# Performance work log

Hardware: AMD Instinct MI355X
Metric: run time of the kernel (lower is better)

Reference implementation:

```python
import jax, jax.numpy as jnp
import numpy as np

G, D, H, O = 8, 1024, 2048, 1024

def _xavier(key, shape):
    # xavier_normal_ on nn.Linear weight [out, in]: std = sqrt(2/(fan_in+fan_out))
    fan_out, fan_in = shape[-2], shape[-1]
    std = float(np.sqrt(2.0 / (fan_in + fan_out)))
    return jax.random.normal(key, shape, dtype=jnp.float32) * std

def setup_inputs() -> dict:
    key = jax.random.key(0)
    kx, kg, ku, kd = jax.random.split(key, 4)
    x = jax.random.normal(kx, (65536, D), dtype=jnp.float32)
    # weights stored per-group in nn.Linear layout [out, in]
    Wg = _xavier(kg, (G, H, D))
    Wu = _xavier(ku, (G, H, D))
    Wd = _xavier(kd, (G, O, H))
    return {"x": x, "Wg": Wg, "Wu": Wu, "Wd": Wd}

def reference(x, Wg, Wu, Wd):
    # x: [B*G, D] -> [B, G, D]
    xb = x.reshape(-1, G, D)
    gate = jnp.einsum('bgd,ghd->bgh', xb, Wg)   # [B, G, H]
    up = jnp.einsum('bgd,ghd->bgh', xb, Wu)     # [B, G, H]
    hidden = jax.nn.silu(gate) * up             # fused SwiGLU
    out = jnp.einsum('bgh,goh->bgo', hidden, Wd)  # [B, G, O]
    return out.reshape(-1, O)
```

## Files before the change

kernel.cpp:

```cpp
#include <hip/hip_runtime.h>


#define GN 8
#define DN 1024
#define HN 2048
#define ON 1024

typedef __attribute__((ext_vector_type(8))) short short8;
typedef __attribute__((ext_vector_type(4))) float f32x4;
typedef __attribute__((ext_vector_type(4))) unsigned int u32x4;

#define BARR() __builtin_amdgcn_s_barrier()
#define WAIT_LGKM0()                                       \
  do {                                                     \
    asm volatile("s_waitcnt lgkmcnt(0)" ::: "memory");     \
    __builtin_amdgcn_sched_barrier(0);                     \
  } while (0)

#define DS128(dst, base, imm)                                                  \
  asm volatile("ds_read_b128 %0, %1 offset:" #imm                              \
               : "=v"(dst)                                                     \
               : "v"((const __attribute__((address_space(3))) unsigned short*)(base)))

__device__ __forceinline__ void async16(const void* g, void* l) {
  __builtin_amdgcn_global_load_lds(
      (const __attribute__((address_space(1))) void*)g,
      (__attribute__((address_space(3))) void*)l, 16, 0, 0);
}

__device__ __forceinline__ unsigned short f2bf(float f) {
  unsigned int u = __float_as_uint(f);
  u += 0x7FFFu + ((u >> 16) & 1u);
  return (unsigned short)(u >> 16);
}

__global__ __launch_bounds__(256) void cvt_f32_bf16(
    const float* __restrict__ in, unsigned short* __restrict__ out, int n) {
  int t = blockIdx.x * 256 + threadIdx.x;
  int i = t * 8;
  if (i >= n) return;
  f32x4 a = *(const f32x4*)(in + i);
  f32x4 b = *(const f32x4*)(in + i + 4);
  u32x4 r;
  r.x = (unsigned)f2bf(a.x) | ((unsigned)f2bf(a.y) << 16);
  r.y = (unsigned)f2bf(a.z) | ((unsigned)f2bf(a.w) << 16);
  r.z = (unsigned)f2bf(b.x) | ((unsigned)f2bf(b.y) << 16);
  r.w = (unsigned)f2bf(b.z) | ((unsigned)f2bf(b.w) << 16);
  *(u32x4*)(out + i) = r;
}

__global__ __launch_bounds__(512, 2) void gemm1_swiglu(
    const unsigned short* __restrict__ Xb, const unsigned short* __restrict__ Wgb,
    const unsigned short* __restrict__ Wub, unsigned short* __restrict__ Hid) {
  extern __shared__ unsigned short sm[];
  unsigned short* sA = sm;
  unsigned short* sG = sm + 32768;
  unsigned short* sU = sm + 49152;

  const int bid = blockIdx.x;
  const int g = bid >> 5;
  const int n0 = ((bid >> 1) & 15) * 128;
  const int mh = bid & 1;

  const int tid = threadIdx.x;
  const int lane = tid & 63;
  const int w = tid >> 6;
  const int wm = w >> 2, wn = w & 3;
  const int fr = lane & 15, fc = lane >> 4;
  const int sR = (fc + ((fr >> 1) & 3)) & 3;

  const unsigned short* aBase[2];
  unsigned short* aDst[2];
#pragma unroll
  for (int j = 0; j < 2; ++j) {
    int R = j * 128 + w * 16 + (lane >> 2);
    int c = ((lane & 3) - ((R >> 1) & 3)) & 3;
    aBase[j] = Xb + ((size_t)((mh * 4096 + R) * 8 + g)) * DN + c * 8;
    aDst[j] = &sA[(j * 128 + w * 16) * 32];
  }
  const unsigned short *gSrc, *uSrc;
  unsigned short *gDst, *uDst;
  {
    int R = w * 16 + (lane >> 2);
    int c = ((lane & 3) - ((R >> 1) & 3)) & 3;
    gSrc = Wgb + ((size_t)(g * HN + n0 + R)) * DN + c * 8;
    uSrc = Wub + ((size_t)(g * HN + n0 + R)) * DN + c * 8;
    gDst = &sG[(w * 16) * 32];
    uDst = &sU[(w * 16) * 32];
  }

  auto stageA = [&](int Tg, int kk) {
    const int buf = (Tg & 1) * 2 + kk;
    const size_t toff = (size_t)(Tg >> 4) * (256u * 8u * DN);
    const int ko = (Tg & 15) * 64 + kk * 32;
#pragma unroll
    for (int j = 0; j < 2; ++j)
      async16(aBase[j] + toff + ko, aDst[j] + buf * 8192);
  };
  auto stageB = [&](int Tg, int kk) {
    const int buf = (Tg & 1) * 2 + kk;
    const int ko = (Tg & 15) * 64 + kk * 32;
    async16(gSrc + ko, gDst + buf * 4096);
    async16(uSrc + ko, uDst + buf * 4096);
  };
  auto readA = [&](int Tg, int kk, short8* a) {
    const unsigned short* p =
        sA + ((Tg & 1) * 2 + kk) * 8192 + (wm * 128 + fr) * 32 + sR * 8;
    DS128(a[0], p, 0);
    DS128(a[1], p, 1024);
    DS128(a[2], p, 2048);
    DS128(a[3], p, 3072);
    DS128(a[4], p, 4096);
    DS128(a[5], p, 5120);
    DS128(a[6], p, 6144);
    DS128(a[7], p, 7168);
  };
  auto readB = [&](const unsigned short* base, int Tg, int kk, short8* b) {
    const unsigned short* p =
        base + ((Tg & 1) * 2 + kk) * 4096 + (wn * 32 + fr) * 32 + sR * 8;
    DS128(b[0], p, 0);
    DS128(b[1], p, 1024);
  };

  f32x4 accg[8][2], accu[8][2];
#pragma unroll
  for (int mi = 0; mi < 8; ++mi)
#pragma unroll
    for (int ni = 0; ni < 2; ++ni) {
      accg[mi][ni] = (f32x4)(0.0f);
      accu[mi][ni] = (f32x4)(0.0f);
    }

  auto mm16 = [&](const short8* a, const short8* b, f32x4(*acc)[2]) {
    __builtin_amdgcn_s_setprio(1);
#pragma unroll
    for (int mi = 0; mi < 8; ++mi)
#pragma unroll
      for (int ni = 0; ni < 2; ++ni)
        acc[mi][ni] = __builtin_amdgcn_mfma_f32_16x16x32_bf16(
            a[mi], b[ni], acc[mi][ni], 0, 0, 0);
    __builtin_amdgcn_s_setprio(0);
  };

  stageA(0, 0); stageB(0, 0); stageA(0, 1); stageB(0, 1);
  stageA(1, 0); stageB(1, 0); stageA(1, 1);
  asm volatile("s_waitcnt vmcnt(6)" ::: "memory");
  BARR();

  short8 af[8], bg[2], bu[2];
  const int q = lane >> 4, cl = lane & 15;
  const int NIT = 128;
#pragma unroll 1
  for (int it = 0; it < NIT; ++it) {
    const int T = 2 * it;
    const bool full = (it + 1 < NIT);
    readA(T, 0, af); readB(sG, T, 0, bg);
    stageB(T + 1, 1);
    BARR();
    WAIT_LGKM0();
    mm16(af, bg, accg);
    BARR();
    readB(sU, T, 0, bu);
    if (full) stageA(T + 2, 0);
    BARR();
    WAIT_LGKM0();
    mm16(af, bu, accu);
    BARR();
    readA(T, 1, af); readB(sG, T, 1, bg);
    if (full) stageB(T + 2, 0);
    BARR();
    WAIT_LGKM0();
    mm16(af, bg, accg);
    BARR();
    readB(sU, T, 1, bu);
    if (full) stageA(T + 2, 1);
    BARR();
    WAIT_LGKM0();
    mm16(af, bu, accu);
    if (full) { asm volatile("s_waitcnt vmcnt(6)" ::: "memory"); }
    else      { asm volatile("s_waitcnt vmcnt(0)" ::: "memory"); }
    BARR();
    readA(T + 1, 0, af); readB(sG, T + 1, 0, bg);
    if (full) stageB(T + 2, 1);
    BARR();
    WAIT_LGKM0();
    mm16(af, bg, accg);
    BARR();
    readB(sU, T + 1, 0, bu);
    if (full) stageA(T + 3, 0);
    BARR();
    WAIT_LGKM0();
    mm16(af, bu, accu);
    BARR();
    readA(T + 1, 1, af); readB(sG, T + 1, 1, bg);
    if (full) stageB(T + 3, 0);
    BARR();
    WAIT_LGKM0();
    mm16(af, bg, accg);
    BARR();
    readB(sU, T + 1, 1, bu);
    if (full) stageA(T + 3, 1);
    BARR();
    WAIT_LGKM0();
    mm16(af, bu, accu);
    if (full) { asm volatile("s_waitcnt vmcnt(6)" ::: "memory"); }
    BARR();
    if ((T & 15) == 14) {
      const int tile = T >> 4;
      const int m0 = (mh * 16 + tile) * 256;
#pragma unroll
      for (int mi = 0; mi < 8; ++mi)
#pragma unroll
        for (int ni = 0; ni < 2; ++ni) {
          int hcol = n0 + wn * 32 + ni * 16 + cl;
#pragma unroll
          for (int i2 = 0; i2 < 4; ++i2) {
            int b = m0 + wm * 128 + mi * 16 + q * 4 + i2;
            float gf = accg[mi][ni][i2];
            float uf = accu[mi][ni][i2];
            float hv = (gf / (1.0f + __expf(-gf))) * uf;
            Hid[((size_t)(b * 8 + g)) * HN + hcol] = f2bf(hv);
          }
          accg[mi][ni] = (f32x4)(0.0f);
          accu[mi][ni] = (f32x4)(0.0f);
        }
    }
  }
}

__global__ __launch_bounds__(512, 2) void gemm2_down(
    const unsigned short* __restrict__ Hid, const unsigned short* __restrict__ Wdb,
    float* __restrict__ Out) {
  extern __shared__ unsigned short sm[];
  unsigned short* sA = sm;
  unsigned short* sB = sm + 32768;

  const int bid = blockIdx.x;
  const int g = bid >> 5;
  const int n0 = ((bid >> 3) & 3) * 256;
  const int mq = bid & 7;

  const int tid = threadIdx.x;
  const int lane = tid & 63;
  const int w = tid >> 6;
  const int wm = w >> 2, wn = w & 3;
  const int fr = lane & 15, fc = lane >> 4;
  const int sR = (fc + ((fr >> 1) & 3)) & 3;

  const unsigned short* aBase[2];
  const unsigned short* bSrc[2];
  unsigned short* aDst[2];
  unsigned short* bDst[2];
#pragma unroll
  for (int j = 0; j < 2; ++j) {
    int R = j * 128 + w * 16 + (lane >> 2);
    int c = ((lane & 3) - ((R >> 1) & 3)) & 3;
    aBase[j] = Hid + ((size_t)((mq * 1024 + R) * 8 + g)) * HN + c * 8;
    bSrc[j] = Wdb + ((size_t)(g * ON + n0 + R)) * HN + c * 8;
    aDst[j] = &sA[(j * 128 + w * 16) * 32];
    bDst[j] = &sB[(j * 128 + w * 16) * 32];
  }

  auto stageA = [&](int Tg, int kk) {
    const int buf = (Tg & 1) * 2 + kk;
    const size_t toff = (size_t)(Tg >> 5) * (256u * 8u * HN);
    const int ko = (Tg & 31) * 64 + kk * 32;
#pragma unroll
    for (int j = 0; j < 2; ++j)
      async16(aBase[j] + toff + ko, aDst[j] + buf * 8192);
  };
  auto stageB = [&](int Tg, int kk) {
    const int buf = (Tg & 1) * 2 + kk;
    const int ko = (Tg & 31) * 64 + kk * 32;
#pragma unroll
    for (int j = 0; j < 2; ++j) async16(bSrc[j] + ko, bDst[j] + buf * 8192);
  };
  auto readA = [&](int Tg, int kk, short8* a) {
    const unsigned short* p =
        sA + ((Tg & 1) * 2 + kk) * 8192 + (wm * 128 + fr) * 32 + sR * 8;
    DS128(a[0], p, 0);
    DS128(a[1], p, 1024);
    DS128(a[2], p, 2048);
    DS128(a[3], p, 3072);
    DS128(a[4], p, 4096);
    DS128(a[5], p, 5120);
    DS128(a[6], p, 6144);
    DS128(a[7], p, 7168);
  };
  auto readB = [&](int Tg, int kk, int nb, short8* b) {
    const unsigned short* p =
        sB + ((Tg & 1) * 2 + kk) * 8192 + (wn * 64 + nb * 16 + fr) * 32 + sR * 8;
    DS128(b[0], p, 0);
    DS128(b[1], p, 1024);
  };

  f32x4 acc[8][4];
#pragma unroll
  for (int mi = 0; mi < 8; ++mi)
#pragma unroll
    for (int ni = 0; ni < 4; ++ni) acc[mi][ni] = (f32x4)(0.0f);

  auto mm16 = [&](const short8* a, const short8* b, int nb) {
    __builtin_amdgcn_s_setprio(1);
#pragma unroll
    for (int mi = 0; mi < 8; ++mi)
#pragma unroll
      for (int nj = 0; nj < 2; ++nj)
        acc[mi][nb + nj] = __builtin_amdgcn_mfma_f32_16x16x32_bf16(
            a[mi], b[nj], acc[mi][nb + nj], 0, 0, 0);
    __builtin_amdgcn_s_setprio(0);
  };

  stageA(0, 0); stageB(0, 0); stageA(0, 1); stageB(0, 1);
  stageA(1, 0); stageB(1, 0); stageA(1, 1);
  asm volatile("s_waitcnt vmcnt(6)" ::: "memory");
  BARR();

  short8 af[8], bf[2];
  const int q = lane >> 4, cl = lane & 15;
  const int NIT = 64;
#pragma unroll 1
  for (int it = 0; it < NIT; ++it) {
    const int T = 2 * it;
    const bool full = (it + 1 < NIT);
    readA(T, 0, af); readB(T, 0, 0, bf);
    stageB(T + 1, 1);
    BARR();
    WAIT_LGKM0();
    mm16(af, bf, 0);
    BARR();
    readB(T, 0, 2, bf);
    if (full) stageA(T + 2, 0);
    BARR();
    WAIT_LGKM0();
    mm16(af, bf, 2);
    BARR();
    readA(T, 1, af); readB(T, 1, 0, bf);
    if (full) stageB(T + 2, 0);
    BARR();
    WAIT_LGKM0();
    mm16(af, bf, 0);
    BARR();
    readB(T, 1, 2, bf);
    if (full) stageA(T + 2, 1);
    BARR();
    WAIT_LGKM0();
    mm16(af, bf, 2);
    if (full) { asm volatile("s_waitcnt vmcnt(6)" ::: "memory"); }
    else      { asm volatile("s_waitcnt vmcnt(0)" ::: "memory"); }
    BARR();
    readA(T + 1, 0, af); readB(T + 1, 0, 0, bf);
    if (full) stageB(T + 2, 1);
    BARR();
    WAIT_LGKM0();
    mm16(af, bf, 0);
    BARR();
    readB(T + 1, 0, 2, bf);
    if (full) stageA(T + 3, 0);
    BARR();
    WAIT_LGKM0();
    mm16(af, bf, 2);
    BARR();
    readA(T + 1, 1, af); readB(T + 1, 1, 0, bf);
    if (full) stageB(T + 3, 0);
    BARR();
    WAIT_LGKM0();
    mm16(af, bf, 0);
    BARR();
    readB(T + 1, 1, 2, bf);
    if (full) stageA(T + 3, 1);
    BARR();
    WAIT_LGKM0();
    mm16(af, bf, 2);
    if (full) { asm volatile("s_waitcnt vmcnt(6)" ::: "memory"); }
    BARR();
    if ((T & 31) == 30) {
      const int tile = T >> 5;
      const int m0 = (mq * 4 + tile) * 256;
#pragma unroll
      for (int mi = 0; mi < 8; ++mi)
#pragma unroll
        for (int ni = 0; ni < 4; ++ni) {
          int o = n0 + wn * 64 + ni * 16 + cl;
#pragma unroll
          for (int i2 = 0; i2 < 4; ++i2) {
            int b = m0 + wm * 128 + mi * 16 + q * 4 + i2;
            Out[((size_t)(b * 8 + g)) * ON + o] = acc[mi][ni][i2];
          }
          acc[mi][ni] = (f32x4)(0.0f);
        }
    }
  }
}

extern "C" void kernel_launch(void* const* d_in, const int* in_sizes, int n_in,
                              void* d_out, int out_size, void* d_ws, size_t ws_size,
                              hipStream_t stream) {
  const float* x  = (const float*)d_in[0];
  const float* Wg = (const float*)d_in[1];
  const float* Wu = (const float*)d_in[2];
  const float* Wd = (const float*)d_in[3];
  float* out = (float*)d_out;

  const int NX = 65536 * 1024;
  const int NW = GN * HN * DN;

  unsigned short* xb = (unsigned short*)d_ws;
  unsigned short* wg = xb + (size_t)NX;
  unsigned short* wu = wg + (size_t)NW;
  unsigned short* wd = wu + (size_t)NW;
  unsigned short* hid = wd + (size_t)NW;

  static bool once = false;
  if (!once) {
    hipFuncSetAttribute((const void*)gemm1_swiglu,
                        hipFuncAttributeMaxDynamicSharedMemorySize, 131072);
    hipFuncSetAttribute((const void*)gemm2_down,
                        hipFuncAttributeMaxDynamicSharedMemorySize, 131072);
    once = true;
  }

  cvt_f32_bf16<<<NX / 8 / 256, 256, 0, stream>>>(x, xb, NX);
  cvt_f32_bf16<<<NW / 8 / 256, 256, 0, stream>>>(Wg, wg, NW);
  cvt_f32_bf16<<<NW / 8 / 256, 256, 0, stream>>>(Wu, wu, NW);
  cvt_f32_bf16<<<NW / 8 / 256, 256, 0, stream>>>(Wd, wd, NW);

  gemm1_swiglu<<<dim3(256), dim3(512), 131072, stream>>>(xb, wg, wu, hid);
  gemm2_down<<<dim3(256), dim3(512), 131072, stream>>>(hid, wd, out);
}
```

Before: 1.356 ms.

## Software-pipeline LDS fragment reads with double-buffered registers and fewer barriers

Both GEMM kernels now double-buffer A fragments in registers (af0/af1). Each MFMA block overlaps with the LDS reads for the next step, using partial lgkmcnt waits instead of a full drain, and the main loop runs one barrier per phase instead of two. Global-to-LDS staging waits now use vmcnt(8) per phase, and tail staging is guarded inside the stage lambdas. The block-index mapping is also changed so neighbouring blocks share the same weight tile across groups and halves, which may improve L2 reuse. The cost is more register pressure from the extra fragment buffers and a tighter hazard protocol around LDS buffer reuse.

Measured after the change: 1.564 ms. 15.3% more time.

```diff
diff --git a/kernel.cpp b/kernel.cpp
--- a/kernel.cpp
+++ b/kernel.cpp
@@ -11,11 +11,13 @@
 typedef __attribute__((ext_vector_type(4))) unsigned int u32x4;
 
 #define BARR() __builtin_amdgcn_s_barrier()
-#define WAIT_LGKM0()                                       \
-  do {                                                     \
-    asm volatile("s_waitcnt lgkmcnt(0)" ::: "memory");     \
-    __builtin_amdgcn_sched_barrier(0);                     \
+#define SCHED0() __builtin_amdgcn_sched_barrier(0)
+#define LGKM(n)                                                \
+  do {                                                         \
+    asm volatile("s_waitcnt lgkmcnt(" #n ")" ::: "memory");    \
+    __builtin_amdgcn_sched_barrier(0);                         \
   } while (0)
+#define VM8() asm volatile("s_waitcnt vmcnt(8)" ::: "memory")
 
 #define DS128(dst, base, imm)                                                  \
   asm volatile("ds_read_b128 %0, %1 offset:" #imm                              \
@@ -58,9 +60,9 @@
   unsigned short* sU = sm + 49152;
 
   const int bid = blockIdx.x;
-  const int g = bid >> 5;
-  const int n0 = ((bid >> 1) & 15) * 128;
+  const int g = (bid & 15) >> 1;
   const int mh = bid & 1;
+  const int n0 = (bid >> 4) * 128;
 
   const int tid = threadIdx.x;
   const int lane = tid & 63;
@@ -89,35 +91,40 @@
     uDst = &sU[(w * 16) * 32];
   }
 
-  auto stageA = [&](int Tg, int kk) {
-    const int buf = (Tg & 1) * 2 + kk;
-    const size_t toff = (size_t)(Tg >> 4) * (256u * 8u * DN);
-    const int ko = (Tg & 15) * 64 + kk * 32;
-#pragma unroll
-    for (int j = 0; j < 2; ++j)
-      async16(aBase[j] + toff + ko, aDst[j] + buf * 8192);
-  };
-  auto stageB = [&](int Tg, int kk) {
-    const int buf = (Tg & 1) * 2 + kk;
-    const int ko = (Tg & 15) * 64 + kk * 32;
+  auto stageA = [&](int t, int kk) {
+    if (t >= 256) return;
+    const int buf = (t & 1) * 2 + kk;
+    const size_t off = (size_t)(t >> 4) * (256u * 8u * DN) + (t & 15) * 64 + kk * 32;
+#pragma unroll
+    for (int j = 0; j < 2; ++j) async16(aBase[j] + off, aDst[j] + buf * 8192);
+  };
+  auto stageB = [&](int t, int kk) {
+    if (t >= 256) return;
+    const int buf = (t & 1) * 2 + kk;
+    const int ko = (t & 15) * 64 + kk * 32;
     async16(gSrc + ko, gDst + buf * 4096);
     async16(uSrc + ko, uDst + buf * 4096);
   };
-  auto readA = [&](int Tg, int kk, short8* a) {
-    const unsigned short* p =
-        sA + ((Tg & 1) * 2 + kk) * 8192 + (wm * 128 + fr) * 32 + sR * 8;
+  auto aPtr = [&](int t, int kk) {
+    return sA + ((t & 1) * 2 + kk) * 8192 + (wm * 128 + fr) * 32 + sR * 8;
+  };
+  auto readAlo = [&](int t, int kk, short8* a) {
+    const unsigned short* p = aPtr(t, kk);
     DS128(a[0], p, 0);
     DS128(a[1], p, 1024);
     DS128(a[2], p, 2048);
     DS128(a[3], p, 3072);
+  };
+  auto readAhi = [&](int t, int kk, short8* a) {
+    const unsigned short* p = aPtr(t, kk);
     DS128(a[4], p, 4096);
     DS128(a[5], p, 5120);
     DS128(a[6], p, 6144);
     DS128(a[7], p, 7168);
   };
-  auto readB = [&](const unsigned short* base, int Tg, int kk, short8* b) {
+  auto readB = [&](const unsigned short* base, int t, int kk, short8* b) {
     const unsigned short* p =
-        base + ((Tg & 1) * 2 + kk) * 4096 + (wn * 32 + fr) * 32 + sR * 8;
+        base + ((t & 1) * 2 + kk) * 4096 + (wn * 32 + fr) * 32 + sR * 8;
     DS128(b[0], p, 0);
     DS128(b[1], p, 1024);
   };
@@ -144,70 +151,66 @@
 
   stageA(0, 0); stageB(0, 0); stageA(0, 1); stageB(0, 1);
   stageA(1, 0); stageB(1, 0); stageA(1, 1);
-  asm volatile("s_waitcnt vmcnt(6)" ::: "memory");
+  asm volatile("s_waitcnt vmcnt(10)" ::: "memory");
   BARR();
-
-  short8 af[8], bg[2], bu[2];
+  short8 af0[8], af1[8], bg[2], bu[2];
+  readAlo(0, 0, af0); readAhi(0, 0, af0); readB(sG, 0, 0, bg);
+
   const int q = lane >> 4, cl = lane & 15;
   const int NIT = 128;
 #pragma unroll 1
   for (int it = 0; it < NIT; ++it) {
     const int T = 2 * it;
-    const bool full = (it + 1 < NIT);
-    readA(T, 0, af); readB(sG, T, 0, bg);
+    BARR(); SCHED0();
     stageB(T + 1, 1);
-    BARR();
-    WAIT_LGKM0();
-    mm16(af, bg, accg);
-    BARR();
-    readB(sU, T, 0, bu);
-    if (full) stageA(T + 2, 0);
-    BARR();
-    WAIT_LGKM0();
-    mm16(af, bu, accu);
-    BARR();
-    readA(T, 1, af); readB(sG, T, 1, bg);
-    if (full) stageB(T + 2, 0);
-    BARR();
-    WAIT_LGKM0();
-    mm16(af, bg, accg);
-    BARR();
-    readB(sU, T, 1, bu);
-    if (full) stageA(T + 2, 1);
-    BARR();
-    WAIT_LGKM0();
-    mm16(af, bu, accu);
-    if (full) { asm volatile("s_waitcnt vmcnt(6)" ::: "memory"); }
-    else      { asm volatile("s_waitcnt vmcnt(0)" ::: "memory"); }
-    BARR();
-    readA(T + 1, 0, af); readB(sG, T + 1, 0, bg);
-    if (full) stageB(T + 2, 1);
-    BARR();
-    WAIT_LGKM0();
-    mm16(af, bg, accg);
-    BARR();
-    readB(sU, T + 1, 0, bu);
-    if (full) stageA(T + 3, 0);
-    BARR();
-    WAIT_LGKM0();
-    mm16(af, bu, accu);
-    BARR();
-    readA(T + 1, 1, af); readB(sG, T + 1, 1, bg);
-    if (full) stageB(T + 3, 0);
-    BARR();
-    WAIT_LGKM0();
-    mm16(af, bg, accg);
-    BARR();
-    readB(sU, T + 1, 1, bu);
-    if (full) stageA(T + 3, 1);
-    BARR();
-    WAIT_LGKM0();
-    mm16(af, bu, accu);
-    if (full) { asm volatile("s_waitcnt vmcnt(6)" ::: "memory"); }
-    BARR();
+    readB(sU, T, 0, bu); readAlo(T, 1, af1);
+    LGKM(6);
+    mm16(af0, bg, accg);
+    VM8();
+    BARR(); SCHED0();
+    stageA(T + 2, 0);
+    readAhi(T, 1, af1); readB(sG, T, 1, bg);
+    LGKM(6);
+    mm16(af0, bu, accu);
+    VM8();
+    BARR(); SCHED0();
+    stageB(T + 2, 0);
+    readB(sU, T, 1, bu); readAlo(T + 1, 0, af0);
+    LGKM(6);
+    mm16(af1, bg, accg);
+    VM8();
+    BARR(); SCHED0();
+    stageA(T + 2, 1);
+    readAhi(T + 1, 0, af0); readB(sG, T + 1, 0, bg);
+    LGKM(6);
+    mm16(af1, bu, accu);
+    VM8();
+    BARR(); SCHED0();
+    stageB(T + 2, 1);
+    readB(sU, T + 1, 0, bu); readAlo(T + 1, 1, af1);
+    LGKM(6);
+    mm16(af0, bg, accg);
+    VM8();
+    BARR(); SCHED0();
+    stageA(T + 3, 0);
+    readAhi(T + 1, 1, af1); readB(sG, T + 1, 1, bg);
+    LGKM(6);
+    mm16(af0, bu, accu);
+    VM8();
+    BARR(); SCHED0();
+    stageB(T + 3, 0);
+    readB(sU, T + 1, 1, bu); readAlo(T + 2, 0, af0);
+    LGKM(6);
+    mm16(af1, bg, accg);
+    VM8();
+    BARR(); SCHED0();
+    stageA(T + 3, 1);
+    readAhi(T + 2, 0, af0); readB(sG, T + 2, 0, bg);
+    LGKM(6);
+    mm16(af1, bu, accu);
+    VM8();
     if ((T & 15) == 14) {
-      const int tile = T >> 4;
-      const int m0 = (mh * 16 + tile) * 256;
+      const int m0 = (mh * 16 + (T >> 4)) * 256;
 #pragma unroll
       for (int mi = 0; mi < 8; ++mi)
 #pragma unroll
@@ -236,9 +239,9 @@
   unsigned short* sB = sm + 32768;
 
   const int bid = blockIdx.x;
-  const int g = bid >> 5;
-  const int n0 = ((bid >> 3) & 3) * 256;
+  const int g = (bid & 63) >> 3;
   const int mq = bid & 7;
+  const int n0 = (bid >> 6) * 256;
 
   const int tid = threadIdx.x;
   const int lane = tid & 63;
@@ -261,35 +264,40 @@
     bDst[j] = &sB[(j * 128 + w * 16) * 32];
   }
 
-  auto stageA = [&](int Tg, int kk) {
-    const int buf = (Tg & 1) * 2 + kk;
-    const size_t toff = (size_t)(Tg >> 5) * (256u * 8u * HN);
-    const int ko = (Tg & 31) * 64 + kk * 32;
-#pragma unroll
-    for (int j = 0; j < 2; ++j)
-      async16(aBase[j] + toff + ko, aDst[j] + buf * 8192);
-  };
-  auto stageB = [&](int Tg, int kk) {
-    const int buf = (Tg & 1) * 2 + kk;
-    const int ko = (Tg & 31) * 64 + kk * 32;
+  auto stageA = [&](int t, int kk) {
+    if (t >= 128) return;
+    const int buf = (t & 1) * 2 + kk;
+    const size_t off = (size_t)(t >> 5) * (256u * 8u * HN) + (t & 31) * 64 + kk * 32;
+#pragma unroll
+    for (int j = 0; j < 2; ++j) async16(aBase[j] + off, aDst[j] + buf * 8192);
+  };
+  auto stageB = [&](int t, int kk) {
+    if (t >= 128) return;
+    const int buf = (t & 1) * 2 + kk;
+    const int ko = (t & 31) * 64 + kk * 32;
 #pragma unroll
     for (int j = 0; j < 2; ++j) async16(bSrc[j] + ko, bDst[j] + buf * 8192);
   };
-  auto readA = [&](int Tg, int kk, short8* a) {
-    const unsigned short* p =
-        sA + ((Tg & 1) * 2 + kk) * 8192 + (wm * 128 + fr) * 32 + sR * 8;
+  auto aPtr = [&](int t, int kk) {
+    return sA + ((t & 1) * 2 + kk) * 8192 + (wm * 128 + fr) * 32 + sR * 8;
+  };
+  auto readAlo = [&](int t, int kk, short8* a) {
+    const unsigned short* p = aPtr(t, kk);
     DS128(a[0], p, 0);
     DS128(a[1], p, 1024);
     DS128(a[2], p, 2048);
     DS128(a[3], p, 3072);
+  };
+  auto readAhi = [&](int t, int kk, short8* a) {
+    const unsigned short* p = aPtr(t, kk);
     DS128(a[4], p, 4096);
     DS128(a[5], p, 5120);
     DS128(a[6], p, 6144);
     DS128(a[7], p, 7168);
   };
-  auto readB = [&](int Tg, int kk, int nb, short8* b) {
+  auto readB = [&](int t, int kk, int nb, short8* b) {
     const unsigned short* p =
-        sB + ((Tg & 1) * 2 + kk) * 8192 + (wn * 64 + nb * 16 + fr) * 32 + sR * 8;
+        sB + ((t & 1) * 2 + kk) * 8192 + (wn * 64 + nb * 16 + fr) * 32 + sR * 8;
     DS128(b[0], p, 0);
     DS128(b[1], p, 1024);
   };
@@ -313,70 +321,66 @@
 
   stageA(0, 0); stageB(0, 0); stageA(0, 1); stageB(0, 1);
   stageA(1, 0); stageB(1, 0); stageA(1, 1);
-  asm volatile("s_waitcnt vmcnt(6)" ::: "memory");
+  asm volatile("s_waitcnt vmcnt(10)" ::: "memory");
   BARR();
-
-  short8 af[8], bf[2];
+  short8 af0[8], af1[8], b01[2], b23[2];
+  readAlo(0, 0, af0); readAhi(0, 0, af0); readB(0, 0, 0, b01);
+
   const int q = lane >> 4, cl = lane & 15;
   const int NIT = 64;
 #pragma unroll 1
   for (int it = 0; it < NIT; ++it) {
     const int T = 2 * it;
-    const bool full = (it + 1 < NIT);
-    readA(T, 0, af); readB(T, 0, 0, bf);
+    BARR(); SCHED0();
     stageB(T + 1, 1);
-    BARR();
-    WAIT_LGKM0();
-    mm16(af, bf, 0);
-    BARR();
-    readB(T, 0, 2, bf);
-    if (full) stageA(T + 2, 0);
-    BARR();
-    WAIT_LGKM0();
-    mm16(af, bf, 2);
-    BARR();
-    readA(T, 1, af); readB(T, 1, 0, bf);
-    if (full) stageB(T + 2, 0);
-    BARR();
-    WAIT_LGKM0();
-    mm16(af, bf, 0);
-    BARR();
-    readB(T, 1, 2, bf);
-    if (full) stageA(T + 2, 1);
-    BARR();
-    WAIT_LGKM0();
-    mm16(af, bf, 2);
-    if (full) { asm volatile("s_waitcnt vmcnt(6)" ::: "memory"); }
-    else      { asm volatile("s_waitcnt vmcnt(0)" ::: "memory"); }
-    BARR();
-    readA(T + 1, 0, af); readB(T + 1, 0, 0, bf);
-    if (full) stageB(T + 2, 1);
-    BARR();
-    WAIT_LGKM0();
-    mm16(af, bf, 0);
-    BARR();
-    readB(T + 1, 0, 2, bf);
-    if (full) stageA(T + 3, 0);
-    BARR();
-    WAIT_LGKM0();
-    mm16(af, bf, 2);
-    BARR();
-    readA(T + 1, 1, af); readB(T + 1, 1, 0, bf);
-    if (full) stageB(T + 3, 0);
-    BARR();
-    WAIT_LGKM0();
-    mm16(af, bf, 0);
-    BARR();
-    readB(T + 1, 1, 2, bf);
-    if (full) stageA(T + 3, 1);
-    BARR();
-    WAIT_LGKM0();
-    mm16(af, bf, 2);
-    if (full) { asm volatile("s_waitcnt vmcnt(6)" ::: "memory"); }
-    BARR();
+    readB(T, 0, 2, b23); readAlo(T, 1, af1);
+    LGKM(6);
+    mm16(af0, b01, 0);
+    VM8();
+    BARR(); SCHED0();
+    stageA(T + 2, 0);
+    readAhi(T, 1, af1); readB(T, 1, 0, b01);
+    LGKM(6);
+    mm16(af0, b23, 2);
+    VM8();
+    BARR(); SCHED0();
+    stageB(T + 2, 0);
+    readB(T, 1, 2, b23); readAlo(T + 1, 0, af0);
+    LGKM(6);
+    mm16(af1, b01, 0);
+    VM8();
+    BARR(); SCHED0();
+    stageA(T + 2, 1);
+    readAhi(T + 1, 0, af0); readB(T + 1, 0, 0, b01);
+    LGKM(6);
+    mm16(af1, b23, 2);
+    VM8();
+    BARR(); SCHED0();
+    stageB(T + 2, 1);
+    readB(T + 1, 0, 2, b23); readAlo(T + 1, 1, af1);
+    LGKM(6);
+    mm16(af0, b01, 0);
+    VM8();
+    BARR(); SCHED0();
+    stageA(T + 3, 0);
+    readAhi(T + 1, 1, af1); readB(T + 1, 1, 0, b01);
+    LGKM(6);
+    mm16(af0, b23, 2);
+    VM8();
+    BARR(); SCHED0();
+    stageB(T + 3, 0);
+    readB(T + 1, 1, 2, b23); readAlo(T + 2, 0, af0);
+    LGKM(6);
+    mm16(af1, b01, 0);
+    VM8();
+    BARR(); SCHED0();
+    stageA(T + 3, 1);
+    readAhi(T + 2, 0, af0); readB(T + 2, 0, 0, b01);
+    LGKM(6);
+    mm16(af1, b23, 2);
+    VM8();
     if ((T & 31) == 30) {
-      const int tile = T >> 5;
-      const int m0 = (mq * 4 + tile) * 256;
+      const int m0 = (mq * 4 + (T >> 5)) * 256;
 #pragma unroll
       for (int mi = 0; mi < 8; ++mi)
 #pragma unroll
```
